# Kernel optimization log

Measured on AMD Instinct MI355X. Metric: run time of the kernel, lower is better.

## Reference

```python
import jax, jax.numpy as jnp
import numpy as np

B, S, H, NH = 2, 2048, 2048, 16
HD = H // NH  # 128
NEG = -1e9


def _rope_tables(seq_len, dim, dtype):
    inv_freq = 1.0 / (10000.0 ** (jnp.arange(0, dim, 2, dtype=jnp.float32) / dim))
    t = jnp.arange(seq_len, dtype=jnp.float32)
    freqs = jnp.einsum('i,j->ij', t, inv_freq)          # [S, dim/2]
    emb = jnp.concatenate([freqs, freqs], axis=-1)      # [S, dim]
    return jnp.cos(emb).astype(dtype), jnp.sin(emb).astype(dtype)


def _rotate_half(x):
    x1, x2 = x[..., : x.shape[-1] // 2], x[..., x.shape[-1] // 2:]
    return jnp.concatenate([-x2, x1], axis=-1)


def setup_inputs() -> dict:
    key = jax.random.key(0)
    ks = jax.random.split(key, 5)
    hidden_states = jax.random.normal(ks[0], (B, S, H), dtype=jnp.float32)
    # causal additive mask [B, S, S]
    causal = jnp.where(jnp.tril(jnp.ones((S, S), dtype=bool)), 0.0, NEG).astype(jnp.float32)
    attention_mask = jnp.broadcast_to(causal, (B, S, S))
    sc = 1.0 / np.sqrt(H)
    Wq = jax.random.normal(ks[1], (H, H), dtype=jnp.float32) * sc
    Wk = jax.random.normal(ks[2], (H, H), dtype=jnp.float32) * sc
    Wv = jax.random.normal(ks[3], (H, H), dtype=jnp.float32) * sc
    Wo = jax.random.normal(ks[4], (H, H), dtype=jnp.float32) * sc
    return {"hidden_states": hidden_states, "attention_mask": attention_mask,
            "Wq": Wq, "Wk": Wk, "Wv": Wv, "Wo": Wo}


def reference(hidden_states, attention_mask, Wq, Wk, Wv, Wo):
    bsz, q_len, _ = hidden_states.shape
    dtype = hidden_states.dtype
    # QKV projections (nn.Linear: x @ W.T), split into heads -> [B, NH, S, HD]
    def proj(W):
        return jnp.einsum('bsh,dh->bsd', hidden_states, W).reshape(bsz, q_len, NH, HD).transpose(0, 2, 1, 3)
    q, k, v = proj(Wq), proj(Wk), proj(Wv)
    cos, sin = _rope_tables(q_len, HD, dtype)            # [S, HD]
    q = q * cos + _rotate_half(q) * sin
    k = k * cos + _rotate_half(k) * sin
    scaling = HD ** -0.5
    scores = jnp.einsum('bhqd,bhkd->bhqk', q, k) * scaling
    scores = scores + attention_mask[:, None, :, :]      # broadcast over heads
    attn = jax.nn.softmax(scores.astype(jnp.float32), axis=-1).astype(dtype)
    out = jnp.einsum('bhqk,bhkd->bhqd', attn, v)         # [B, NH, S, HD]
    out = out.transpose(0, 2, 1, 3).reshape(bsz, q_len, H)
    return jnp.einsum('bsh,dh->bsd', out, Wo)
```

## Files before the change

kernel.cpp:

```cpp
#include <hip/hip_runtime.h>
#include <hip/hip_bf16.h>
#include <math.h>

#define B_  2
#define S_  2048
#define H_  2048
#define NH_ 16
#define HD_ 128
#define M_  (B_*S_)

typedef __bf16 bf16_t;
typedef _Float16 f16_t;
typedef __bf16 bf16x8 __attribute__((ext_vector_type(8)));
typedef __bf16 bf16x4 __attribute__((ext_vector_type(4)));
typedef _Float16 f16x4 __attribute__((ext_vector_type(4)));
typedef float  f32x4  __attribute__((ext_vector_type(4)));

__device__ __forceinline__ f32x4 mfma_bf16_32(bf16x8 a, bf16x8 b, f32x4 c) {
  return __builtin_amdgcn_mfma_f32_16x16x32_bf16(a, b, c, 0, 0, 0);
}
__device__ __forceinline__ f32x4 mfma_f16_16(f16x4 a, f16x4 b, f32x4 c) {
  return __builtin_amdgcn_mfma_f32_16x16x16f16(a, b, c, 0, 0, 0);
}
__device__ __forceinline__ void gl_lds16(const void* g, void* l) {
  __builtin_amdgcn_global_load_lds((const __attribute__((address_space(1))) void*)g,
                                   (__attribute__((address_space(3))) void*)l, 16, 0, 0);
}
#define WAITCNT_VM(n) { asm volatile("" ::: "memory"); \
                        __builtin_amdgcn_s_waitcnt(((n) & 0xF) | 0x70 | 0xF00 | (((n) >> 4) << 14)); \
                        asm volatile("" ::: "memory"); }
#define BARRIER()     { asm volatile("" ::: "memory"); __builtin_amdgcn_s_barrier(); \
                        asm volatile("" ::: "memory"); }

__global__ void cvt_all(const float* __restrict__ hs, const float* __restrict__ wq,
                        const float* __restrict__ wk, const float* __restrict__ wv,
                        const float* __restrict__ wo, bf16_t* __restrict__ hs_b,
                        bf16_t* __restrict__ wqkv, bf16_t* __restrict__ wo_b) {
  int i = (blockIdx.x * 256 + threadIdx.x) * 4;
  const float* src;
  bf16_t* dst;
  if (i < 8388608)        { src = hs + i;              dst = hs_b + i; }
  else if (i < 12582912)  { src = wq + (i - 8388608);  dst = wqkv + (i - 8388608); }
  else if (i < 16777216)  { src = wk + (i - 12582912); dst = wqkv + (i - 8388608); }
  else if (i < 20971520)  { src = wv + (i - 16777216); dst = wqkv + (i - 8388608); }
  else                    { src = wo + (i - 20971520); dst = wo_b + (i - 20971520); }
  float4 v = *(const float4*)src;
  bf16x4 o;
  o[0] = (bf16_t)v.x; o[1] = (bf16_t)v.y; o[2] = (bf16_t)v.z; o[3] = (bf16_t)v.w;
  *(bf16x4*)dst = o;
}

template<int MODE>
__global__ __launch_bounds__(256, 3)
void gemm_mfma(const bf16_t* __restrict__ A, const bf16_t* __restrict__ Bt,
               bf16_t* __restrict__ outQ, bf16_t* __restrict__ outK,
               f16_t* __restrict__ outV, float* __restrict__ outF, int K) {
  __shared__ bf16_t sS[128 * 128];
  bf16_t* const sA = sS;
  bf16_t* const sB = sS + 128 * 64;
  const int tid  = threadIdx.x;
  const int lane = tid & 63;
  const int w    = tid >> 6;
  const int col  = lane & 15;
  const int quad = lane >> 4;
  const int w_m  = (w & 1) * 64;
  const int w_n  = (w >> 1) * 64;
  const int m_blk = blockIdx.y * 128;
  const int n_blk = blockIdx.x * 128;

  const int srow   = lane >> 3;
  const int schunk = (lane & 7) ^ (lane >> 3);

  const bf16_t* Abase = A  + (size_t)m_blk * K;
  const bf16_t* Bbase = Bt + (size_t)n_blk * K;

  f32x4 acc[4][4] = {};

  for (int kk = 0; kk < K; kk += 64) {
    __syncthreads();
#pragma unroll
    for (int p = 0; p < 4; ++p) {
      int seg = w * 4 + p;
      int row = seg * 8 + srow;
      gl_lds16(Abase + (size_t)row * K + kk + schunk * 8, &sA[seg * 512]);
      gl_lds16(Bbase + (size_t)row * K + kk + schunk * 8, &sB[seg * 512]);
    }
    __syncthreads();
#pragma unroll
    for (int kc = 0; kc < 2; ++kc) {
      bf16x8 af[4], bfr[4];
      const int cs = (kc * 4 + quad) ^ (col & 7);
#pragma unroll
      for (int i = 0; i < 4; ++i) {
        af[i]  = *(const bf16x8*)&sA[(w_m + i * 16 + col) * 64 + cs * 8];
        bfr[i] = *(const bf16x8*)&sB[(w_n + i * 16 + col) * 64 + cs * 8];
      }
#pragma unroll
      for (int mi = 0; mi < 4; ++mi)
#pragma unroll
        for (int ni = 0; ni < 4; ++ni)
          acc[mi][ni] = mfma_bf16_32(af[mi], bfr[ni], acc[mi][ni]);
    }
  }

  const int sel = n_blk >> 11;
  if (MODE == 0 && sel == 2) {
#pragma unroll
    for (int mi = 0; mi < 4; ++mi)
#pragma unroll
      for (int ni = 0; ni < 4; ++ni) {
        int m0 = m_blk + w_m + mi * 16 + quad * 4;
        int n  = n_blk + w_n + ni * 16 + col;
        int n_l = n & (H_ - 1);
        int head = n_l >> 7, hd = n_l & (HD_ - 1);
        int b = m0 >> 11, s0 = m0 & (S_ - 1);
        int bh = b * NH_ + head;
        int frag = (bh * 32 + (s0 >> 6)) * 32 + (hd >> 4) * 4 + ((s0 >> 4) & 3);
        int lane2 = ((s0 >> 2) & 3) * 16 + (hd & 15);
        f16x4 o;
#pragma unroll
        for (int r = 0; r < 4; ++r) o[r] = (f16_t)acc[mi][ni][r];
        *(f16x4*)&outV[(size_t)frag * 256 + lane2 * 4] = o;
      }
  } else if (MODE == 0) {
    __syncthreads();
#pragma unroll
    for (int mi = 0; mi < 4; ++mi)
#pragma unroll
      for (int ni = 0; ni < 4; ++ni) {
        int lm0 = w_m + mi * 16 + quad * 4;
        int ln  = w_n + ni * 16 + col;
#pragma unroll
        for (int r = 0; r < 4; ++r) {
          int lm = lm0 + r;
          sS[lm * 128 + (ln ^ ((lm & 7) << 3))] = (bf16_t)acc[mi][ni][r];
        }
      }
    __syncthreads();
    const int row  = tid >> 1;
    const int half = tid & 1;
    const int m    = m_blk + row;
    const int b    = m >> 11, s = m & (S_ - 1);
    const int head = (n_blk & (H_ - 1)) >> 7;
    const int bh   = b * NH_ + head;
    const int swz  = (row & 7) << 3;
    const int kt = s >> 6, t = (s >> 4) & 3;
    bf16_t* qwr   = outQ + ((size_t)bh * S_ + s) * HD_ + half * 32;
    bf16_t* kbase = outK + ((size_t)(bh * 32 + kt) * 16) * 512;
#pragma unroll
    for (int k = 0; k < 4; ++k) {
      int e1 = row * 128 + ((half * 32 + k * 8) ^ swz);
      bf16x8 x1 = *(const bf16x8*)&sS[e1];
      bf16x8 x2 = *(const bf16x8*)&sS[e1 + 64];
      bf16x8 o1, o2;
#pragma unroll
      for (int j = 0; j < 8; ++j) {
        int d = half * 32 + k * 8 + j;
        float ang = (float)s * exp2f(-(float)d * (13.287712379549449f / 64.f));
        float cc, sn;
        sincosf(ang, &sn, &cc);
        float a1 = (float)x1[j], a2 = (float)x2[j];
        o1[j] = (bf16_t)(a1 * cc - a2 * sn);
        o2[j] = (bf16_t)(a2 * cc + a1 * sn);
      }
      if (sel == 0) {
        *(bf16x8*)(qwr + k * 8)      = o1;
        *(bf16x8*)(qwr + 64 + k * 8) = o2;
      } else {
        int lane_ = k * 16 + (s & 15);
        *(bf16x8*)(kbase + (size_t)(t * 4 + half) * 512 + lane_ * 8)     = o1;
        *(bf16x8*)(kbase + (size_t)(t * 4 + half + 2) * 512 + lane_ * 8) = o2;
      }
    }
  } else {
#pragma unroll
    for (int mi = 0; mi < 4; ++mi)
#pragma unroll
      for (int ni = 0; ni < 4; ++ni)
#pragma unroll
        for (int r = 0; r < 4; ++r) {
          int m = m_blk + w_m + mi * 16 + quad * 4 + r;
          int n = n_blk + w_n + ni * 16 + col;
          outF[(size_t)m * H_ + n] = acc[mi][ni][r];
        }
  }
}

__global__ __launch_bounds__(256, 4)
void flash_attn(const bf16_t* __restrict__ Q, const bf16_t* __restrict__ Kp,
                const f16_t* __restrict__ Vp, bf16_t* __restrict__ Out) {
  __shared__ bf16_t sK[8192];
  __shared__ f16_t  sV[8192];
  const int lane = threadIdx.x & 63;
  const int col  = lane & 15;
  const int quad = lane >> 4;
  const int w    = threadIdx.x >> 6;

  const int c = blockIdx.x & 7, g = blockIdx.x >> 3;
  const int g2 = (g + (blockIdx.y >> 3)) & 3;
  const int qt = (g2 == 0) ? c : (g2 == 1) ? 15 - c : (g2 == 2) ? 16 + c : 31 - c;
  const int bh = blockIdx.y;
  const int ktmax = qt;

  const bf16_t* KpB = Kp + (size_t)bh * 32 * 8192;
  const f16_t*  VpB = Vp + (size_t)bh * 32 * 8192;

  auto stageK = [&](int kt) {
#pragma unroll
    for (int r = 0; r < 4; ++r) {
      int seg = r * 4 + w;
      gl_lds16(KpB + (size_t)kt * 8192 + seg * 512 + lane * 8, &sK[seg * 512]);
    }
  };
  auto stageV = [&](int kt) {
#pragma unroll
    for (int r = 0; r < 4; ++r) {
      int seg = r * 4 + w;
      gl_lds16(VpB + (size_t)kt * 8192 + seg * 512 + lane * 8, &sV[seg * 512]);
    }
  };

  const float scale2 = 0.12751744154f;
  const bf16_t* Qrow = Q + ((size_t)bh * S_ + qt * 64 + w * 16 + col) * HD_;
  bf16x8 qf[4];
#pragma unroll
  for (int kc = 0; kc < 4; ++kc) {
    qf[kc] = *(const bf16x8*)(Qrow + kc * 32 + quad * 8);
#pragma unroll
    for (int j = 0; j < 8; ++j) qf[kc][j] = (bf16_t)((float)qf[kc][j] * scale2);
  }

  f32x4 oacc[8] = {};
  float m_i = -1e30f, l_i = 0.f;

  stageK(0);
  stageV(0);
  WAITCNT_VM(4)
  BARRIER();

  for (int kt = 0; kt <= ktmax; ++kt) {
    f32x4 st[4] = {};
    __builtin_amdgcn_s_setprio(1);
#pragma unroll
    for (int kc = 0; kc < 4; ++kc)
#pragma unroll
      for (int t = 0; t < 4; ++t) {
        bf16x8 kf = *(const bf16x8*)&sK[(t * 4 + kc) * 512 + lane * 8];
        st[t] = mfma_bf16_32(kf, qf[kc], st[t]);
      }
    __builtin_amdgcn_s_setprio(0);

    if (kt == ktmax) {
      int ql = w * 16 + col;
#pragma unroll
      for (int t = 0; t < 4; ++t)
#pragma unroll
        for (int r = 0; r < 4; ++r)
          if (t * 16 + quad * 4 + r > ql) st[t][r] = -1e30f;
    }

    float mx = st[0][0];
#pragma unroll
    for (int t = 0; t < 4; ++t)
#pragma unroll
      for (int r = 0; r < 4; ++r) mx = fmaxf(mx, st[t][r]);
    mx = fmaxf(mx, __shfl_xor(mx, 16, 64));
    mx = fmaxf(mx, __shfl_xor(mx, 32, 64));
    if (__ballot(mx - m_i > 8.0f)) {
      float mn = fmaxf(m_i, mx);
      float alpha = exp2f(m_i - mn);
#pragma unroll
      for (int dt = 0; dt < 8; ++dt)
#pragma unroll
        for (int r = 0; r < 4; ++r) oacc[dt][r] *= alpha;
      l_i *= alpha;
      m_i = mn;
    }

    float sum = 0.f;
    f16x4 pf[4];
#pragma unroll
    for (int t = 0; t < 4; ++t)
#pragma unroll
      for (int r = 0; r < 4; ++r) {
        float pv = exp2f(st[t][r] - m_i);
        sum += pv;
        pf[t][r] = (f16_t)pv;
      }
    sum += __shfl_xor(sum, 16, 64);
    sum += __shfl_xor(sum, 32, 64);
    l_i += sum;

    WAITCNT_VM(0)
    BARRIER();

    if (kt < ktmax) stageK(kt + 1);

    __builtin_amdgcn_s_setprio(1);
#pragma unroll
    for (int t = 0; t < 4; ++t)
#pragma unroll
      for (int dt = 0; dt < 8; ++dt) {
        f16x4 vf = *(const f16x4*)&sV[(dt * 4 + t) * 256 + lane * 4];
        oacc[dt] = mfma_f16_16(vf, pf[t], oacc[dt]);
      }
    __builtin_amdgcn_s_setprio(0);

    if (kt < ktmax) {
      BARRIER();
      stageV(kt + 1);
      WAITCNT_VM(4)
      BARRIER();
    }
  }

  float inv = 1.0f / l_i;
  int b = bh >> 4, h = bh & (NH_ - 1);
  int qg = qt * 64 + w * 16 + col;
  bf16_t* Orow = Out + ((size_t)b * S_ + qg) * H_ + h * HD_;
#pragma unroll
  for (int dt = 0; dt < 8; ++dt) {
    bf16x4 o4;
#pragma unroll
    for (int r = 0; r < 4; ++r) o4[r] = (bf16_t)(oacc[dt][r] * inv);
    *(bf16x4*)(Orow + dt * 16 + quad * 4) = o4;
  }
}

extern "C" void kernel_launch(void* const* d_in, const int* in_sizes, int n_in,
                              void* d_out, int out_size, void* d_ws, size_t ws_size,
                              hipStream_t stream) {
  const float* hs = (const float*)d_in[0];
  const float* Wq = (const float*)d_in[2];
  const float* Wk = (const float*)d_in[3];
  const float* Wv = (const float*)d_in[4];
  const float* Wo = (const float*)d_in[5];
  float* out = (float*)d_out;

  char* ws = (char*)d_ws;
  size_t off = 0;
  auto alloc = [&](size_t bytes) -> void* {
    void* p = ws + off;
    off += (bytes + 255) & ~(size_t)255;
    return p;
  };
  bf16_t* hs_b  = (bf16_t*)alloc((size_t)M_ * H_ * 2);
  bf16_t* wqkv  = (bf16_t*)alloc((size_t)3 * H_ * H_ * 2);
  bf16_t* wo_b  = (bf16_t*)alloc((size_t)H_ * H_ * 2);
  bf16_t* Qbuf  = (bf16_t*)alloc((size_t)M_ * H_ * 2);
  bf16_t* Kp    = (bf16_t*)alloc((size_t)M_ * H_ * 2);
  f16_t*  Vp    = (f16_t*)alloc((size_t)M_ * H_ * 2);
  bf16_t* attn  = (bf16_t*)alloc((size_t)M_ * H_ * 2);

  cvt_all<<<24576, 256, 0, stream>>>(hs, Wq, Wk, Wv, Wo, hs_b, wqkv, wo_b);

  gemm_mfma<0><<<dim3(48, 32), 256, 0, stream>>>(hs_b, wqkv, Qbuf, Kp,
                                                 Vp, nullptr, H_);

  flash_attn<<<dim3(32, 32), 256, 0, stream>>>(Qbuf, Kp, Vp, attn);

  gemm_mfma<1><<<dim3(16, 32), 256, 0, stream>>>(attn, wo_b, nullptr, nullptr,
                                                 nullptr, out, H_);
}
```

Before: 368.1 us.

## Apply RoPE directly from MFMA accumulators, skipping the LDS staging epilogue

Each wave's N columns are remapped so that it holds both rotate-half partners (d and d+64) in its own registers. RoPE can then run straight from the accumulators, with no LDS transpose and no extra barriers. sincosf is replaced by the hardware sin/cos instructions on a range-reduced revolution count, which lowers transcendental cost. The trade-off is that Q/K stores become scalar bf16 writes instead of 16-byte vectors, and the hardware trig may lose precision at large angles.

```diff
diff --git a/kernel.cpp b/kernel.cpp
--- a/kernel.cpp
+++ b/kernel.cpp
@@ -55,16 +55,15 @@
 void gemm_mfma(const bf16_t* __restrict__ A, const bf16_t* __restrict__ Bt,
                bf16_t* __restrict__ outQ, bf16_t* __restrict__ outK,
                f16_t* __restrict__ outV, float* __restrict__ outF, int K) {
-  __shared__ bf16_t sS[128 * 128];
-  bf16_t* const sA = sS;
-  bf16_t* const sB = sS + 128 * 64;
+  __shared__ bf16_t sA[128 * 64];
+  __shared__ bf16_t sB[128 * 64];
   const int tid  = threadIdx.x;
   const int lane = tid & 63;
   const int w    = tid >> 6;
   const int col  = lane & 15;
   const int quad = lane >> 4;
   const int w_m  = (w & 1) * 64;
-  const int w_n  = (w >> 1) * 64;
+  const int w_n2 = (w >> 1) * 32;
   const int m_blk = blockIdx.y * 128;
   const int n_blk = blockIdx.x * 128;
 
@@ -93,7 +92,7 @@
 #pragma unroll
       for (int i = 0; i < 4; ++i) {
         af[i]  = *(const bf16x8*)&sA[(w_m + i * 16 + col) * 64 + cs * 8];
-        bfr[i] = *(const bf16x8*)&sB[(w_n + i * 16 + col) * 64 + cs * 8];
+        bfr[i] = *(const bf16x8*)&sB[(w_n2 + (i & 1) * 16 + (i >> 1) * 64 + col) * 64 + cs * 8];
       }
 #pragma unroll
       for (int mi = 0; mi < 4; ++mi)
@@ -110,7 +109,7 @@
 #pragma unroll
       for (int ni = 0; ni < 4; ++ni) {
         int m0 = m_blk + w_m + mi * 16 + quad * 4;
-        int n  = n_blk + w_n + ni * 16 + col;
+        int n  = n_blk + w_n2 + (ni & 1) * 16 + (ni >> 1) * 64 + col;
         int n_l = n & (H_ - 1);
         int head = n_l >> 7, hd = n_l & (HD_ - 1);
         int b = m0 >> 11, s0 = m0 & (S_ - 1);
@@ -123,64 +122,48 @@
         *(f16x4*)&outV[(size_t)frag * 256 + lane2 * 4] = o;
       }
   } else if (MODE == 0) {
-    __syncthreads();
-#pragma unroll
-    for (int mi = 0; mi < 4; ++mi)
-#pragma unroll
-      for (int ni = 0; ni < 4; ++ni) {
-        int lm0 = w_m + mi * 16 + quad * 4;
-        int ln  = w_n + ni * 16 + col;
-#pragma unroll
-        for (int r = 0; r < 4; ++r) {
-          int lm = lm0 + r;
-          sS[lm * 128 + (ln ^ ((lm & 7) << 3))] = (bf16_t)acc[mi][ni][r];
-        }
-      }
-    __syncthreads();
-    const int row  = tid >> 1;
-    const int half = tid & 1;
-    const int m    = m_blk + row;
-    const int b    = m >> 11, s = m & (S_ - 1);
     const int head = (n_blk & (H_ - 1)) >> 7;
-    const int bh   = b * NH_ + head;
-    const int swz  = (row & 7) << 3;
-    const int kt = s >> 6, t = (s >> 4) & 3;
-    bf16_t* qwr   = outQ + ((size_t)bh * S_ + s) * HD_ + half * 32;
-    bf16_t* kbase = outK + ((size_t)(bh * 32 + kt) * 16) * 512;
-#pragma unroll
-    for (int k = 0; k < 4; ++k) {
-      int e1 = row * 128 + ((half * 32 + k * 8) ^ swz);
-      bf16x8 x1 = *(const bf16x8*)&sS[e1];
-      bf16x8 x2 = *(const bf16x8*)&sS[e1 + 64];
-      bf16x8 o1, o2;
-#pragma unroll
-      for (int j = 0; j < 8; ++j) {
-        int d = half * 32 + k * 8 + j;
-        float ang = (float)s * exp2f(-(float)d * (13.287712379549449f / 64.f));
-        float cc, sn;
-        sincosf(ang, &sn, &cc);
-        float a1 = (float)x1[j], a2 = (float)x2[j];
-        o1[j] = (bf16_t)(a1 * cc - a2 * sn);
-        o2[j] = (bf16_t)(a2 * cc + a1 * sn);
-      }
-      if (sel == 0) {
-        *(bf16x8*)(qwr + k * 8)      = o1;
-        *(bf16x8*)(qwr + 64 + k * 8) = o2;
-      } else {
-        int lane_ = k * 16 + (s & 15);
-        *(bf16x8*)(kbase + (size_t)(t * 4 + half) * 512 + lane_ * 8)     = o1;
-        *(bf16x8*)(kbase + (size_t)(t * 4 + half + 2) * 512 + lane_ * 8) = o2;
-      }
-    }
-  } else {
-#pragma unroll
-    for (int mi = 0; mi < 4; ++mi)
-#pragma unroll
-      for (int ni = 0; ni < 4; ++ni)
+#pragma unroll
+    for (int ni = 0; ni < 2; ++ni) {
+      const int d = w_n2 + ni * 16 + col;
+      const float rf = exp2f(-(float)d * 0.20762050593046f - 2.6514961294723187f);
+#pragma unroll
+      for (int mi = 0; mi < 4; ++mi) {
 #pragma unroll
         for (int r = 0; r < 4; ++r) {
           int m = m_blk + w_m + mi * 16 + quad * 4 + r;
-          int n = n_blk + w_n + ni * 16 + col;
+          int b = m >> 11, s = m & (S_ - 1);
+          int bh = b * NH_ + head;
+          float rev = (float)s * rf;
+          rev -= floorf(rev);
+          float cc = __builtin_amdgcn_cosf(rev);
+          float sn = __builtin_amdgcn_sinf(rev);
+          float x1 = acc[mi][ni][r], x2 = acc[mi][ni + 2][r];
+          float o1 = x1 * cc - x2 * sn;
+          float o2 = x2 * cc + x1 * sn;
+          if (sel == 0) {
+            bf16_t* qwr = outQ + ((size_t)bh * S_ + s) * HD_;
+            qwr[d]      = (bf16_t)o1;
+            qwr[d + 64] = (bf16_t)o2;
+          } else {
+            int kt = s >> 6, t = (s >> 4) & 3;
+            int lane_ = ((d >> 3) & 3) * 16 + (s & 15);
+            bf16_t* kbase = outK + ((size_t)(bh * 32 + kt) * 16) * 512;
+            kbase[(size_t)(t * 4 + (d >> 5)) * 512 + lane_ * 8 + (d & 7)]     = (bf16_t)o1;
+            kbase[(size_t)(t * 4 + (d >> 5) + 2) * 512 + lane_ * 8 + (d & 7)] = (bf16_t)o2;
+          }
+        }
+      }
+    }
+  } else {
+#pragma unroll
+    for (int mi = 0; mi < 4; ++mi)
+#pragma unroll
+      for (int ni = 0; ni < 4; ++ni)
+#pragma unroll
+        for (int r = 0; r < 4; ++r) {
+          int m = m_blk + w_m + mi * 16 + quad * 4 + r;
+          int n = n_blk + w_n2 + (ni & 1) * 16 + (ni >> 1) * 64 + col;
           outF[(size_t)m * H_ + n] = acc[mi][ni][r];
         }
   }
```

Result: no change. 372.4 us (median of 2 runs) (+1.2%).
